# Optimization experiments

Measured on AMD Instinct MI355X. Metric: run time of the kernel, lower is better.

Reference implementation:

```python
import jax, jax.numpy as jnp
import numpy as np
from jax import lax

B, S, L, H, D_IN, W = 128, 64, 137, 128, 64, 256  # batch, segments, logsig_dim, hidden, input_dim, vf_width


def setup_inputs() -> dict:
    key = jax.random.key(0)
    ks = jax.random.split(key, 12)
    rn = lambda k, s, sc: jax.random.normal(k, s, dtype=jnp.float32) * sc
    return {
        "times": jnp.arange(S + 1, dtype=jnp.float32),
        "logsig": rn(ks[0], (B, S, L), 0.1),
        "initial": rn(ks[1], (B, D_IN), 1.0),
        "in_w": rn(ks[2], (D_IN, H), 0.12),
        "in_b": rn(ks[3], (H,), 0.05),
        "h1_w": rn(ks[4], (H, W), 0.09),
        "h1_b": rn(ks[5], (W,), 0.05),
        "h2_w": rn(ks[6], (W, W), 0.06),
        "h2_b": rn(ks[7], (W,), 0.05),
        "vo_w": rn(ks[8], (W, W), 0.06),
        "vo_b": rn(ks[9], (W,), 0.05),
        "ml_w": rn(ks[10], (W, H * (L - 1)), 0.02),
        "ml_b": rn(ks[11], (H * (L - 1),), 0.01),
    }


def reference(times, logsig, initial, in_w, in_b, h1_w, h1_b, h2_w, h2_b, vo_w, vo_b, ml_w, ml_b):
    intervals = times                 # [S+1]; forward requires times == registered intervals
    coeffs = logsig[:, :, 1:]         # [B, S, L-1] (first logsig channel dropped)
    h0 = initial @ in_w + in_b        # [B, H]

    def func(t, y):
        # searchsorted + clamp, exactly as in the torch module
        idx = jnp.clip(jnp.searchsorted(intervals, t, side='left'), 1, S)
        dt = intervals[idx] - intervals[idx - 1]
        coeff = jnp.take(coeffs, idx - 1, axis=1)        # [B, L-1]
        h = jax.nn.relu(y @ h1_w + h1_b)                 # vf MLP (vf_depth-1 = 2 hidden layers)
        h = jax.nn.relu(h @ h2_w + h2_b)
        h = jnp.tanh(h @ vo_w + vo_b)                    # final tanh activation
        vf = (h @ ml_w + ml_b).reshape(B, H, L - 1)      # [B, H, L-1]
        return jnp.einsum('bhd,bd->bh', vf, coeff) / dt  # [B, H]

    def step(y, n):
        # one fixed-size Heun (RK2) step from intervals[n] to intervals[n+1]
        t0, t1 = intervals[n], intervals[n + 1]
        dt = t1 - t0
        k1 = func(t0, y)
        k2 = func(t1, y + dt * k1)
        y1 = y + 0.5 * dt * (k1 + k2)
        return y1, y1

    _, ys = lax.scan(step, h0, jnp.arange(S))            # ys: [S, B, H]
    features = jnp.concatenate([h0[:, None, :], jnp.swapaxes(ys, 0, 1)], axis=1)  # [B, S+1, H]
    return features, features[:, -1]
```

## Files before the change

kernel.cpp:

```cpp
#include <hip/hip_runtime.h>
#include <hip/hip_bf16.h>


#define BB 128
#define SS 64
#define LL 137
#define HH 128
#define DIN 64
#define WW 256
#define DD 136
#define KP 160
#define NC 32768
#define OUT2_OFF ((size_t)BB*(SS+1)*HH)

typedef __hip_bfloat16 bf16;
typedef __attribute__((ext_vector_type(8))) short short8;
typedef __attribute__((ext_vector_type(4))) float f32x4;
typedef _Float16 h2t __attribute__((ext_vector_type(2)));

__device__ __forceinline__ bf16 f2bf(float x){ return __float2bfloat16(x); }

__device__ __forceinline__ float fdot2u(unsigned w, unsigned y, float acc){
#if __has_builtin(__builtin_amdgcn_fdot2)
  return __builtin_amdgcn_fdot2(__builtin_bit_cast(h2t, w),
                                __builtin_bit_cast(h2t, y), acc, false);
#else
  h2t a = __builtin_bit_cast(h2t, w), b2 = __builtin_bit_cast(h2t, y);
  return acc + (float)a[0]*(float)b2[0] + (float)a[1]*(float)b2[1];
#endif
}
__device__ __forceinline__ float dot8(uint4 w, uint4 y, float acc){
  acc = fdot2u(w.x, y.x, acc);
  acc = fdot2u(w.y, y.y, acc);
  acc = fdot2u(w.z, y.z, acc);
  acc = fdot2u(w.w, y.w, acc);
  return acc;
}

__device__ __forceinline__ float fast_tanh(float x){
  float e = __expf(2.f*x);
#if __has_builtin(__builtin_amdgcn_rcpf)
  float r = __builtin_amdgcn_rcpf(e + 1.f);
#else
  float r = 1.f/(e + 1.f);
#endif
  return 1.f - 2.f*r;
}

__global__ void prep_coeff(const float* __restrict__ logsig, bf16* __restrict__ cA){
  int m = blockIdx.x;
  int d = threadIdx.x;
  int a = m >> 7, b = m & 127;
  float v = 0.0f;
  if (d < DD) v = logsig[(size_t)(b*SS + a)*LL + 1 + d];
  int kk = d >> 5, q = (d >> 3) & 3, jj = d & 7;
  cA[(((size_t)(kk*4 + q))*8192 + m)*8 + jj] = f2bf(v);
}

__global__ void prep_btt(const float* __restrict__ mlw, bf16* __restrict__ btt){
  int c = blockIdx.x;
  int d = threadIdx.x;
  int w = ((c >> 10) << 3) | (c & 7);
  int h = (c >> 3) & 127;
  float v = 0.0f;
  if (d < DD) v = mlw[(size_t)w*(HH*DD) + h*DD + d];
  int kk = d >> 5, q = (d >> 3) & 3, jj = d & 7;
  btt[(((size_t)(kk*4 + q))*NC + c)*8 + jj] = f2bf(v);
}

__global__ void prep_packw(const float* __restrict__ src, uint4* __restrict__ dst){
  int c = blockIdx.x, j = threadIdx.x;
  union { _Float16 h[8]; uint4 v; } u;
  #pragma unroll
  for (int r = 0; r < 8; ++r) u.h[r] = (_Float16)src[(size_t)(c*8+r)*WW + j];
  dst[c*WW + j] = u.v;
}

__global__ void abias_kernel(const float* __restrict__ mlb, const float* __restrict__ logsig,
                             float* __restrict__ Abias){
  int a = blockIdx.x, b = blockIdx.y;
  int h = threadIdx.x;
  __shared__ float cf[DD];
  for (int d = h; d < DD; d += HH) cf[d] = logsig[(size_t)(b*SS + a)*LL + 1 + d];
  __syncthreads();
  float acc = 0.f;
  const float* mb = mlb + (size_t)h*DD;
  #pragma unroll 8
  for (int d = 0; d < DD; ++d) acc += cf[d] * mb[d];
  Abias[((size_t)a*BB + b)*HH + h] = acc;
}

__global__ __launch_bounds__(512) void agemm_kernel(const bf16* __restrict__ cA,
                                                    const bf16* __restrict__ btt,
                                                    _Float16* __restrict__ As, int mAbs0){
  __shared__ __align__(16) char smb[81920];
  short* sm = (short*)smb;
  int mt = blockIdx.x, nt = blockIdx.y;
  int t = threadIdx.x, lane = t & 63, wid = t >> 6;
  int mBlockAbs = mAbs0 + mt*128;
  int c0 = nt*128;
  int mW = (wid & 3)*32, cW = (wid >> 2)*64;
  const uint4* aK = (const uint4*)cA;
  const uint4* bK = (const uint4*)btt;

  uint4 va[5], vb[5];
  #pragma unroll
  for (int r = 0; r < 5; ++r){
    int lin = t + r*512;
    int kq = lin >> 7;
    int row = lin & 127;
    va[r] = aK[(size_t)kq*8192 + mBlockAbs + row];
    vb[r] = bK[(size_t)kq*NC + c0 + row];
  }
  #pragma unroll
  for (int r = 0; r < 5; ++r){
    int lin = t + r*512;
    *(uint4*)(smb + lin*16) = va[r];
    *(uint4*)(smb + 40960 + lin*16) = vb[r];
  }
  __syncthreads();

  f32x4 acc[2][4];
  #pragma unroll
  for (int i = 0; i < 2; ++i)
    #pragma unroll
    for (int j = 0; j < 4; ++j)
      acc[i][j] = (f32x4){0.f,0.f,0.f,0.f};

  const int mr = lane & 15, q = lane >> 4;
  #pragma unroll
  for (int kk = 0; kk < 5; ++kk){
    short8 af[2], bfr[4];
    #pragma unroll
    for (int mi = 0; mi < 2; ++mi)
      af[mi]  = *(const short8*)(smb + ((size_t)((kk*4+q)*128) + mW + mi*16 + mr)*16);
    #pragma unroll
    for (int ci = 0; ci < 4; ++ci)
      bfr[ci] = *(const short8*)(smb + 40960 + ((size_t)((kk*4+q)*128) + cW + ci*16 + mr)*16);
    #pragma unroll
    for (int mi = 0; mi < 2; ++mi)
      #pragma unroll
      for (int ci = 0; ci < 4; ++ci)
        acc[mi][ci] = __builtin_amdgcn_mfma_f32_16x16x32_bf16(af[mi], bfr[ci], acc[mi][ci], 0, 0, 0);
  }
  __syncthreads();

  #pragma unroll
  for (int mi = 0; mi < 2; ++mi)
    #pragma unroll
    for (int ci = 0; ci < 4; ++ci){
      int col = cW + ci*16 + mr;
      #pragma unroll
      for (int r = 0; r < 4; ++r){
        int row = mW + mi*16 + q*4 + r;
        _Float16 hv = (_Float16)acc[mi][ci][r];
        sm[row*136 + col] = *(short*)&hv;
      }
    }
  __syncthreads();
  int mLocBlock = mt*128;
  #pragma unroll
  for (int rep = 0; rep < 4; ++rep){
    int idx = t + rep*512;
    int row = idx >> 4, seg = idx & 15;
    uint4 v = *(const uint4*)&sm[row*136 + seg*8];
    *(uint4*)(As + (size_t)(mLocBlock + row)*NC + c0 + seg*8) = v;
  }
}

__device__ __forceinline__ float nrde_func(
    int j, int q, int h, int q4,
    const uint4 (&w1r)[8], const uint4 (&w2r)[16], const uint4 (&vor)[16],
    const uint4 (&ar)[8], float ab,
    const _Float16* yh, _Float16* h1h, _Float16* h2h, _Float16* h3h,
    float b1, float b2, float bv, float inv_dtf)
{
  {
    const uint4* yp = (const uint4*)yh + (q << 3);
    float a0 = 0.f, a1 = 0.f;
    #pragma unroll
    for (int cc = 0; cc < 8; cc += 2){
      a0 = dot8(w1r[cc],   yp[cc],   a0);
      a1 = dot8(w1r[cc+1], yp[cc+1], a1);
    }
    float acc = a0 + a1;
    acc += __shfl_xor(acc, 32);
    if (q == 0){ float v = b1 + acc; h1h[j] = (_Float16)(v > 0.f ? v : 0.f); }
  }
  __syncthreads();
  {
    const uint4* hp = (const uint4*)h1h + (q << 4);
    float a0 = 0.f, a1 = 0.f, a2 = 0.f, a3 = 0.f;
    #pragma unroll
    for (int cc = 0; cc < 16; cc += 4){
      a0 = dot8(w2r[cc],   hp[cc],   a0);
      a1 = dot8(w2r[cc+1], hp[cc+1], a1);
      a2 = dot8(w2r[cc+2], hp[cc+2], a2);
      a3 = dot8(w2r[cc+3], hp[cc+3], a3);
    }
    float acc = (a0 + a1) + (a2 + a3);
    acc += __shfl_xor(acc, 32);
    if (q == 0){ float v = b2 + acc; h2h[j] = (_Float16)(v > 0.f ? v : 0.f); }
  }
  __syncthreads();
  {
    const uint4* hp = (const uint4*)h2h + (q << 4);
    float a0 = 0.f, a1 = 0.f, a2 = 0.f, a3 = 0.f;
    #pragma unroll
    for (int cc = 0; cc < 16; cc += 4){
      a0 = dot8(vor[cc],   hp[cc],   a0);
      a1 = dot8(vor[cc+1], hp[cc+1], a1);
      a2 = dot8(vor[cc+2], hp[cc+2], a2);
      a3 = dot8(vor[cc+3], hp[cc+3], a3);
    }
    float acc = (a0 + a1) + (a2 + a3);
    acc += __shfl_xor(acc, 32);
    if (q == 0) h3h[j] = (_Float16)fast_tanh(bv + acc);
  }
  __syncthreads();
  {
    const uint4* hp = (const uint4*)h3h + (q4 << 3);
    float a0 = 0.f, a1 = 0.f;
    #pragma unroll
    for (int cc = 0; cc < 8; cc += 2){
      a0 = dot8(ar[cc],   hp[cc],   a0);
      a1 = dot8(ar[cc+1], hp[cc+1], a1);
    }
    float acc = a0 + a1;
    acc += __shfl_xor(acc, 16);
    acc += __shfl_xor(acc, 32);
    return (acc + ab) * inv_dtf;
  }
}

__global__ __launch_bounds__(512, 2) void scan_kernel(
    const float* __restrict__ times, const float* __restrict__ initial,
    const float* __restrict__ in_w, const float* __restrict__ in_b,
    const float* __restrict__ h1_b, const float* __restrict__ h2_b,
    const float* __restrict__ vo_b,
    const uint4* __restrict__ wp1, const uint4* __restrict__ wp2,
    const uint4* __restrict__ wpv,
    const _Float16* __restrict__ As, const float* __restrict__ Abias,
    float* __restrict__ y_state, float* __restrict__ out,
    int s0, int s1, int aBase)
{
  __shared__ __align__(16) char smem[4608];
  _Float16* yh  = (_Float16*)(smem);
  _Float16* h1h = (_Float16*)(smem + 512);
  _Float16* h2h = (_Float16*)(smem + 1536);
  _Float16* h3h = (_Float16*)(smem + 2560);
  float*    yv  = (float*)(smem + 3584);

  const int b = blockIdx.x, t = threadIdx.x;
  const int wave = t >> 6, lane = t & 63;
  const int j  = (wave << 5) | (lane & 31);
  const int q  = lane >> 5;
  const int h  = (wave << 4) | (lane & 15);
  const int q4 = lane >> 4;
  const bool tail = (lane >> 4) == 0;

  uint4 w1r[8], w2r[16], vor[16];
  #pragma unroll
  for (int cc = 0; cc < 8; ++cc)  w1r[cc] = wp1[(size_t)((q << 3) + cc)*WW + j];
  #pragma unroll
  for (int cc = 0; cc < 16; ++cc) w2r[cc] = wp2[(size_t)((q << 4) + cc)*WW + j];
  #pragma unroll
  for (int cc = 0; cc < 16; ++cc) vor[cc] = wpv[(size_t)((q << 4) + cc)*WW + j];
  const float b1 = h1_b[j], b2 = h2_b[j], bv = vo_b[j];

  if (s0 == 0){
    if (t < HH){
      float acc = in_b[t];
      for (int i = 0; i < DIN; ++i)
        acc += initial[b*DIN + i] * in_w[(size_t)i*HH + t];
      yv[t] = acc; yh[t] = (_Float16)acc;
      out[(size_t)b*(SS+1)*HH + t] = acc;
    }
  } else if (t < HH){
    float v = y_state[b*HH + t];
    yv[t] = v; yh[t] = (_Float16)v;
  }

  uint4 ar[8];
  float ab;
  {
    int a1s = (s0 >= 1) ? (s0 - 1) : 0;
    const uint4* Ap = (const uint4*)(As + ((size_t)(a1s - aBase)*BB + b)*NC);
    #pragma unroll
    for (int cc = 0; cc < 8; ++cc) ar[cc] = Ap[(size_t)((q4 << 3) + cc)*HH + h];
    ab = Abias[((size_t)a1s*BB + b)*HH + h];
  }
  __syncthreads();

  for (int n = s0; n < s1; ++n){
    float dt = times[n+1] - times[n];
    int idx1 = (n >= 1) ? n : 1;
    float inv1 = 1.f/(times[idx1] - times[idx1-1]);
    float invd = 1.f/dt;

    float k1 = nrde_func(j, q, h, q4, w1r, w2r, vor, ar, ab,
                         yh, h1h, h2h, h3h, b1, b2, bv, inv1);
    if (tail) yh[h] = (_Float16)(yv[h] + dt*k1);
    __syncthreads();

    {
      const uint4* Ap = (const uint4*)(As + ((size_t)(n - aBase)*BB + b)*NC);
      #pragma unroll
      for (int cc = 0; cc < 8; ++cc) ar[cc] = Ap[(size_t)((q4 << 3) + cc)*HH + h];
      ab = Abias[((size_t)n*BB + b)*HH + h];
    }
    float k2 = nrde_func(j, q, h, q4, w1r, w2r, vor, ar, ab,
                         yh, h1h, h2h, h3h, b1, b2, bv, invd);
    if (tail){
      float ynew = yv[h] + 0.5f*dt*(k1 + k2);
      yv[h] = ynew; yh[h] = (_Float16)ynew;
      out[((size_t)b*(SS+1) + (n+1))*HH + h] = ynew;
    }
    __syncthreads();
  }

  if (tail){
    y_state[b*HH + h] = yv[h];
    if (s1 == SS) out[OUT2_OFF + (size_t)b*HH + h] = yv[h];
  }
}

extern "C" void kernel_launch(void* const* d_in, const int* in_sizes, int n_in,
                              void* d_out, int out_size, void* d_ws, size_t ws_size,
                              hipStream_t stream)
{
  (void)in_sizes; (void)n_in; (void)out_size;
  const float* times   = (const float*)d_in[0];
  const float* logsig  = (const float*)d_in[1];
  const float* initial = (const float*)d_in[2];
  const float* in_w    = (const float*)d_in[3];
  const float* in_b    = (const float*)d_in[4];
  const float* h1_w    = (const float*)d_in[5];
  const float* h1_b    = (const float*)d_in[6];
  const float* h2_w    = (const float*)d_in[7];
  const float* h2_b    = (const float*)d_in[8];
  const float* vo_w    = (const float*)d_in[9];
  const float* vo_b    = (const float*)d_in[10];
  const float* ml_w    = (const float*)d_in[11];
  const float* ml_b    = (const float*)d_in[12];
  float* out = (float*)d_out;

  char* ws = (char*)d_ws;
  size_t off = 0;
  bf16* cA      = (bf16*)(ws + off); off += (size_t)8192*KP*2;
  bf16* btt     = (bf16*)(ws + off); off += (size_t)NC*KP*2;
  float* Abias  = (float*)(ws + off); off += (size_t)SS*BB*HH*4;
  float* y_state= (float*)(ws + off); off += (size_t)BB*HH*4;
  uint4* wp1    = (uint4*)(ws + off); off += (size_t)16*WW*16;
  uint4* wp2    = (uint4*)(ws + off); off += (size_t)32*WW*16;
  uint4* wpv    = (uint4*)(ws + off); off += (size_t)32*WW*16;
  _Float16* As  = (_Float16*)(ws + off);
  size_t perA = (size_t)BB*HH*WW*2;
  size_t avail = (ws_size > off) ? (ws_size - off) : 0;
  int C = (int)(avail / perA);
  if (C > SS) C = SS;
  if (C < 2) return;

  prep_coeff<<<8192, 160, 0, stream>>>(logsig, cA);
  prep_btt<<<NC, 160, 0, stream>>>(ml_w, btt);
  abias_kernel<<<dim3(SS, BB), HH, 0, stream>>>(ml_b, logsig, Abias);
  prep_packw<<<16, WW, 0, stream>>>(h1_w, wp1);
  prep_packw<<<32, WW, 0, stream>>>(h2_w, wp2);
  prep_packw<<<32, WW, 0, stream>>>(vo_w, wpv);

  int s = 0, aB = 0;
  while (s < SS){
    int cc = SS - aB; if (cc > C) cc = C;
    agemm_kernel<<<dim3(cc, 256), 512, 0, stream>>>(cA, btt, As, aB*128);
    int sEnd = aB + cc; if (sEnd > SS) sEnd = SS;
    scan_kernel<<<BB, 512, 0, stream>>>(times, initial, in_w, in_b,
        h1_b, h2_b, vo_b, wp1, wp2, wpv, As, Abias, y_state, out, s, sEnd, aB);
    s = sEnd;
    aB = sEnd - 1;
  }
}
```

Before: 609.8 us.

## Fuse prep kernels and remap agemm blocks for XCD-local L2 reuse

Merges the abias computation into the coefficient prep kernel so logsig is read once, and collapses the three weight-packing launches into a single launch. It also flattens the agemm grid and remaps block IDs so that each XCD (blocks assigned round-robin by flat&7) handles a contiguous range of 32 N-tiles. Those blocks then share btt tiles in that XCD's L2. This cuts launch overhead and redundant global reads, but relies on the assumed round-robin XCD dispatch order.

New measurement: 614.4 us. Within noise of the previous version (+0.8%).

```diff
diff --git a/kernel.cpp b/kernel.cpp
--- a/kernel.cpp
+++ b/kernel.cpp
@@ -47,14 +47,24 @@
   return 1.f - 2.f*r;
 }
 
-__global__ void prep_coeff(const float* __restrict__ logsig, bf16* __restrict__ cA){
+__global__ void prep_ca(const float* __restrict__ logsig, const float* __restrict__ mlb,
+                        bf16* __restrict__ cA, float* __restrict__ Abias){
   int m = blockIdx.x;
   int d = threadIdx.x;
   int a = m >> 7, b = m & 127;
+  __shared__ float cf[DD];
   float v = 0.0f;
-  if (d < DD) v = logsig[(size_t)(b*SS + a)*LL + 1 + d];
+  if (d < DD){ v = logsig[(size_t)(b*SS + a)*LL + 1 + d]; cf[d] = v; }
   int kk = d >> 5, q = (d >> 3) & 3, jj = d & 7;
   cA[(((size_t)(kk*4 + q))*8192 + m)*8 + jj] = f2bf(v);
+  __syncthreads();
+  if (d < HH){
+    float acc = 0.f;
+    const float* mb = mlb + (size_t)d*DD;
+    #pragma unroll 8
+    for (int dd = 0; dd < DD; ++dd) acc += cf[dd] * mb[dd];
+    Abias[((size_t)a*BB + b)*HH + d] = acc;
+  }
 }
 
 __global__ void prep_btt(const float* __restrict__ mlw, bf16* __restrict__ btt){
@@ -68,34 +78,31 @@
   btt[(((size_t)(kk*4 + q))*NC + c)*8 + jj] = f2bf(v);
 }
 
-__global__ void prep_packw(const float* __restrict__ src, uint4* __restrict__ dst){
-  int c = blockIdx.x, j = threadIdx.x;
+__global__ void prep_packw_all(const float* __restrict__ h1w, const float* __restrict__ h2w,
+                               const float* __restrict__ vow,
+                               uint4* __restrict__ wp1, uint4* __restrict__ wp2,
+                               uint4* __restrict__ wpv){
+  int blk = blockIdx.x, j = threadIdx.x;
+  const float* src; uint4* dst; int c;
+  if (blk < 16)      { src = h1w; dst = wp1; c = blk; }
+  else if (blk < 48) { src = h2w; dst = wp2; c = blk - 16; }
+  else               { src = vow; dst = wpv; c = blk - 48; }
   union { _Float16 h[8]; uint4 v; } u;
   #pragma unroll
   for (int r = 0; r < 8; ++r) u.h[r] = (_Float16)src[(size_t)(c*8+r)*WW + j];
   dst[c*WW + j] = u.v;
 }
 
-__global__ void abias_kernel(const float* __restrict__ mlb, const float* __restrict__ logsig,
-                             float* __restrict__ Abias){
-  int a = blockIdx.x, b = blockIdx.y;
-  int h = threadIdx.x;
-  __shared__ float cf[DD];
-  for (int d = h; d < DD; d += HH) cf[d] = logsig[(size_t)(b*SS + a)*LL + 1 + d];
-  __syncthreads();
-  float acc = 0.f;
-  const float* mb = mlb + (size_t)h*DD;
-  #pragma unroll 8
-  for (int d = 0; d < DD; ++d) acc += cf[d] * mb[d];
-  Abias[((size_t)a*BB + b)*HH + h] = acc;
-}
-
 __global__ __launch_bounds__(512) void agemm_kernel(const bf16* __restrict__ cA,
                                                     const bf16* __restrict__ btt,
-                                                    _Float16* __restrict__ As, int mAbs0){
+                                                    _Float16* __restrict__ As,
+                                                    int mAbs0, int cc){
   __shared__ __align__(16) char smb[81920];
   short* sm = (short*)smb;
-  int mt = blockIdx.x, nt = blockIdx.y;
+  int flat = blockIdx.x;
+  int xcd = flat & 7, rr = flat >> 3;
+  int mt = rr % cc, ntl = rr / cc;
+  int nt = xcd*32 + ntl;
   int t = threadIdx.x, lane = t & 63, wid = t >> 6;
   int mBlockAbs = mAbs0 + mt*128;
   int c0 = nt*128;
@@ -361,17 +368,14 @@
   if (C > SS) C = SS;
   if (C < 2) return;
 
-  prep_coeff<<<8192, 160, 0, stream>>>(logsig, cA);
+  prep_ca<<<8192, 160, 0, stream>>>(logsig, ml_b, cA, Abias);
   prep_btt<<<NC, 160, 0, stream>>>(ml_w, btt);
-  abias_kernel<<<dim3(SS, BB), HH, 0, stream>>>(ml_b, logsig, Abias);
-  prep_packw<<<16, WW, 0, stream>>>(h1_w, wp1);
-  prep_packw<<<32, WW, 0, stream>>>(h2_w, wp2);
-  prep_packw<<<32, WW, 0, stream>>>(vo_w, wpv);
+  prep_packw_all<<<80, WW, 0, stream>>>(h1_w, h2_w, vo_w, wp1, wp2, wpv);
 
   int s = 0, aB = 0;
   while (s < SS){
     int cc = SS - aB; if (cc > C) cc = C;
-    agemm_kernel<<<dim3(cc, 256), 512, 0, stream>>>(cA, btt, As, aB*128);
+    agemm_kernel<<<cc*256, 512, 0, stream>>>(cA, btt, As, aB*128, cc);
     int sEnd = aB + cc; if (sEnd > SS) sEnd = SS;
     scan_kernel<<<BB, 512, 0, stream>>>(times, initial, in_w, in_b,
         h1_b, h2_b, vo_b, wp1, wp2, wpv, As, Abias, y_state, out, s, sEnd, aB);
```
